# Kernel tuning notes

Hardware: AMD Instinct MI355X
Metric: run time of the kernel (lower is better)

The kernel has to match this reference:

```python
import jax, jax.numpy as jnp
import numpy as np

NB_CLASSES = 1024
SZ_EMBED = 128
N_SAMPLES = 262144
MRG = 0.1
ALPHA = 32.0


def l2_norm(x):
    # matches torch l2_norm: divide by sqrt(sum(x^2, dim=1) + 1e-12)
    return x / jnp.sqrt(jnp.sum(x * x, axis=1, keepdims=True) + 1e-12)


def setup_inputs() -> dict:
    key = jax.random.key(0)
    k1, k2, k3 = jax.random.split(key, 3)
    X = jax.random.normal(k1, (N_SAMPLES, SZ_EMBED), dtype=jnp.float32)
    proxies = jax.random.normal(k2, (NB_CLASSES, SZ_EMBED), dtype=jnp.float32)
    T = jax.random.randint(k3, (N_SAMPLES,), 0, NB_CLASSES)
    return {"X": X, "proxies": proxies, "T": T}


def reference(X, proxies, T):
    # cosine similarities: [N, C]
    cos = l2_norm(X) @ l2_norm(proxies).T
    # on-device one-hot replaces the numpy binarize roundtrip
    P_one_hot = jax.nn.one_hot(T, NB_CLASSES, dtype=cos.dtype)  # [N, C]
    pos_exp_w = jnp.exp(-ALPHA * (cos - MRG)) * P_one_hot
    neg_exp_w = jnp.exp(ALPHA * (cos + MRG)) * (1.0 - P_one_hot)
    P_sim_sum = pos_exp_w.sum(axis=0)  # [C]
    N_sim_sum = neg_exp_w.sum(axis=0)  # [C]
    num_valid = (P_one_hot.sum(axis=0) != 0).sum().astype(cos.dtype)
    pos_term = jnp.where(
        num_valid > 0,
        jnp.log1p(P_sim_sum).sum() / jnp.maximum(num_valid, 1.0),
        jnp.zeros((), cos.dtype),
    )
    neg_term = jnp.log1p(N_sim_sum).sum() / NB_CLASSES
    loss = pos_term + neg_term
    return jnp.stack([loss, pos_term, neg_term])
```

## Files before the change

### kernel.cpp

```cpp
#include <hip/hip_runtime.h>
#include <math.h>

#define NB_CLASSES 1024
#define SZ_EMBED 128
#define N_SAMPLES 262144
#define MTILE 64
#define CTILE 64
#define NBLOCKS (N_SAMPLES / MTILE)
#define XSTRIDE 136

typedef __bf16 v8bf __attribute__((ext_vector_type(8)));
typedef float v4f __attribute__((ext_vector_type(4)));
typedef float v2f __attribute__((ext_vector_type(2)));

#define EXP_A 46.16624130844683f
#define EXP_B 4.616624130844683f

#define SMEM_BYTES 36096

__device__ __forceinline__ unsigned short f2bf(float f) {
    union { float f; unsigned u; } v; v.f = f;
    unsigned u = v.u;
    unsigned rounding = 0x7FFFu + ((u >> 16) & 1u);
    return (unsigned short)((u + rounding) >> 16);
}
__device__ __forceinline__ float bfbits_lo(unsigned u) {
    union { unsigned u; float f; } v; v.u = u << 16; return v.f;
}
__device__ __forceinline__ float bfbits_hi(unsigned u) {
    union { unsigned u; float f; } v; v.u = u & 0xffff0000u; return v.f;
}

__global__ __launch_bounds__(256) void norm_proxies_kernel(
    const float* __restrict__ proxies, unsigned short* __restrict__ pn,
    float* __restrict__ pg) {
    if (blockIdx.x < 8) pg[blockIdx.x * 256 + threadIdx.x] = 0.f;
    int wv = threadIdx.x >> 6;
    int lane = threadIdx.x & 63;
    int row = blockIdx.x * 4 + wv;
    const float* src = proxies + (size_t)row * SZ_EMBED + lane * 2;
    float2 x = *(const float2*)src;
    float ss = x.x * x.x + x.y * x.y;
    #pragma unroll
    for (int off = 32; off; off >>= 1) ss += __shfl_xor(ss, off);
    float inv = rsqrtf(ss + 1e-12f);
    unsigned pk = (unsigned)f2bf(x.x * inv) | ((unsigned)f2bf(x.y * inv) << 16);
    *(unsigned*)(pn + (size_t)row * SZ_EMBED + lane * 2) = pk;
}

__global__ __launch_bounds__(256) void main_kernel(
    const float* __restrict__ X, const int* __restrict__ T,
    const unsigned short* __restrict__ Pn,
    float* __restrict__ partial_neg, float* __restrict__ pos_g,
    float* __restrict__ negd_g) {
    __shared__ __align__(16) char smem[SMEM_BYTES];
    unsigned short* xtile = (unsigned short*)smem;
    float (*psum)[4] = (float(*)[4])(smem + 17408);
    float (*dsum)[4] = (float(*)[4])(smem + 18432);
    int* tT = (int*)(smem + 19456);

    const int t = threadIdx.x;
    const int lane = t & 63;
    const int wv = t >> 6;
    const int quad = lane >> 4;
    const int l15 = lane & 15;
    const int sample_base = blockIdx.x * MTILE;
    const int row = t >> 2, part = t & 3;
    const char* PnB = (const char*)Pn;

#define STAGE(tc, b) do {                                                      \
        char* lb_ = smem + ((b) ? 0 : 19712) + wv * 4096;                      \
        _Pragma("unroll")                                                      \
        for (int c_ = 0; c_ < 4; ++c_) {                                       \
            int rw_ = c_ * 4 + (lane >> 4);                                    \
            const char* g_ = PnB + ((size_t)((tc) * 64 + wv * 16 + rw_)) * 256 \
                             + (((lane & 15) * 16) ^ ((rw_ & 7) << 4));        \
            __builtin_amdgcn_global_load_lds(                                  \
                (__attribute__((address_space(1))) const void*)g_,             \
                (__attribute__((address_space(3))) void*)(lb_ + c_ * 1024),    \
                16, 0, 0);                                                     \
        }                                                                      \
    } while (0)

    STAGE(0, 0);

    {
        const float4* src = (const float4*)(X + (size_t)(sample_base + row) * SZ_EMBED + part * 32);
        float4 r[8];
        float ss = 0.f;
        #pragma unroll
        for (int j = 0; j < 8; ++j) {
            r[j] = src[j];
            ss += r[j].x * r[j].x + r[j].y * r[j].y + r[j].z * r[j].z + r[j].w * r[j].w;
        }
        psum[row][part] = ss;
        if (t < MTILE) tT[t] = T[sample_base + t];
        __syncthreads();
        float inv = rsqrtf(psum[row][0] + psum[row][1] + psum[row][2] + psum[row][3] + 1e-12f);
        unsigned short* dst = xtile + row * XSTRIDE + part * 32;
        #pragma unroll
        for (int j = 0; j < 8; ++j) {
            uint2 pk;
            pk.x = (unsigned)f2bf(r[j].x * inv) | ((unsigned)f2bf(r[j].y * inv) << 16);
            pk.y = (unsigned)f2bf(r[j].z * inv) | ((unsigned)f2bf(r[j].w * inv) << 16);
            *(uint2*)(dst + j * 4) = pk;
        }
        int lbl = tT[row];
        const unsigned short* prow = Pn + (size_t)lbl * SZ_EMBED + part * 32;
        float d = 0.f;
        #pragma unroll
        for (int j = 0; j < 4; ++j) {
            uint4 pv = *(const uint4*)(prow + j * 8);
            float4 xa = r[2 * j], xb = r[2 * j + 1];
            d += bfbits_lo(pv.x) * xa.x + bfbits_hi(pv.x) * xa.y;
            d += bfbits_lo(pv.y) * xa.z + bfbits_hi(pv.y) * xa.w;
            d += bfbits_lo(pv.z) * xb.x + bfbits_hi(pv.z) * xb.y;
            d += bfbits_lo(pv.w) * xb.z + bfbits_hi(pv.w) * xb.w;
        }
        dsum[row][part] = d * inv;
        __syncthreads();
        if (part == 0) {
            int lbl2 = tT[row];
            float dd = dsum[row][0] + dsum[row][1] + dsum[row][2] + dsum[row][3];
            float dp = __builtin_amdgcn_exp2f(fmaf(dd, -EXP_A, EXP_B));
            float dn = __builtin_amdgcn_exp2f(fmaf(dd,  EXP_A, EXP_B));
            atomicAdd(&pos_g[lbl2], dp);
            atomicAdd(&negd_g[lbl2], dn);
        }
    }

    v8bf afrag[4][4];
    #pragma unroll
    for (int ri = 0; ri < 4; ++ri)
        #pragma unroll
        for (int kc = 0; kc < 4; ++kc)
            afrag[ri][kc] = *(const v8bf*)(xtile + (ri * 16 + l15) * XSTRIDE + kc * 32 + quad * 8);

    __syncthreads();

    float* nrow = partial_neg + (size_t)blockIdx.x * NB_CLASSES + wv * 16 + l15;
    const int bswz = ((l15 & 7) << 4);
    const int browoff = (wv * 16 + l15) * 256;

    #pragma unroll
    for (int ct = 0; ct < NB_CLASSES / CTILE; ++ct) {
        const int cur = ct & 1;
        if (ct < NB_CLASSES / CTILE - 1) {
            STAGE(ct + 1, cur ^ 1);
            asm volatile("s_waitcnt vmcnt(5)" ::: "memory");
        } else {
            asm volatile("s_waitcnt vmcnt(1)" ::: "memory");
        }
        __builtin_amdgcn_sched_barrier(0);

        const char* bbase = smem + (cur ? 0 : 19712) + browoff;
        v8bf bfrag[4];
        #pragma unroll
        for (int kc = 0; kc < 4; ++kc)
            bfrag[kc] = *(const v8bf*)(bbase + ((kc * 64 + quad * 16) ^ bswz));

        v4f zero = {0.f, 0.f, 0.f, 0.f};
        v4f acc[4] = {zero, zero, zero, zero};
        #pragma unroll
        for (int kc = 0; kc < 4; ++kc)
            #pragma unroll
            for (int ri = 0; ri < 4; ++ri)
                acc[ri] = __builtin_amdgcn_mfma_f32_16x16x32_bf16(afrag[ri][kc], bfrag[kc], acc[ri], 0, 0, 0);

        v2f e2[8];
        #pragma unroll
        for (int ri = 0; ri < 4; ++ri) {
            float a0 = __builtin_amdgcn_exp2f(fmaf(acc[ri][0], EXP_A, EXP_B));
            float a1 = __builtin_amdgcn_exp2f(fmaf(acc[ri][1], EXP_A, EXP_B));
            float a2 = __builtin_amdgcn_exp2f(fmaf(acc[ri][2], EXP_A, EXP_B));
            float a3 = __builtin_amdgcn_exp2f(fmaf(acc[ri][3], EXP_A, EXP_B));
            e2[ri * 2]     = (v2f){a0, a1};
            e2[ri * 2 + 1] = (v2f){a2, a3};
        }
        #pragma unroll
        for (int s2 = 4; s2; s2 >>= 1)
            #pragma unroll
            for (int j = 0; j < s2; ++j)
                e2[j] += e2[j + s2];
        float v = e2[0].x + e2[0].y;
        v += __shfl_xor(v, 16);
        v += __shfl_xor(v, 32);
        if (quad == 0) nrow[ct * CTILE] = v;
    }
#undef STAGE
}

__global__ __launch_bounds__(256) void row_reduce_kernel(float* __restrict__ partial_neg) {
    const int t = threadIdx.x;
    const int g = blockIdx.x >> 2, q = blockIdx.x & 3;
    float* base = partial_neg + (size_t)g * 64 * NB_CLASSES + q * 256 + t;
    float s = 0.f;
    #pragma unroll 8
    for (int r = 0; r < 64; ++r) s += base[(size_t)r * NB_CLASSES];
    base[0] = s;
}

__global__ __launch_bounds__(256) void finalize_kernel(
    const float* __restrict__ partial_neg, const float* __restrict__ pos_g,
    const float* __restrict__ negd_g, float* __restrict__ out) {
    int t = threadIdx.x;
    float4 ns = {0.f, 0.f, 0.f, 0.f};
    #pragma unroll 8
    for (int r = 0; r < 64; ++r) {
        float4 vn = *(const float4*)(partial_neg + (size_t)r * 64 * NB_CLASSES + 4 * t);
        ns.x += vn.x; ns.y += vn.y; ns.z += vn.z; ns.w += vn.w;
    }
    float4 nd = *(const float4*)(negd_g + 4 * t);
    ns.x -= nd.x; ns.y -= nd.y; ns.z -= nd.z; ns.w -= nd.w;
    float4 ps = *(const float4*)(pos_g + 4 * t);
    float lp_pos = log1pf(ps.x) + log1pf(ps.y) + log1pf(ps.z) + log1pf(ps.w);
    float lp_neg = log1pf(ns.x) + log1pf(ns.y) + log1pf(ns.z) + log1pf(ns.w);
    float valid = (ps.x != 0.f) + (ps.y != 0.f) + (ps.z != 0.f) + (ps.w != 0.f);
    #pragma unroll
    for (int off = 32; off; off >>= 1) {
        lp_pos += __shfl_xor(lp_pos, off);
        lp_neg += __shfl_xor(lp_neg, off);
        valid  += __shfl_xor(valid, off);
    }
    __shared__ float s[3][4];
    int wv = t >> 6, lane = t & 63;
    if (lane == 0) { s[0][wv] = lp_pos; s[1][wv] = lp_neg; s[2][wv] = valid; }
    __syncthreads();
    if (t == 0) {
        float P = s[0][0] + s[0][1] + s[0][2] + s[0][3];
        float Ng = s[1][0] + s[1][1] + s[1][2] + s[1][3];
        float V = s[2][0] + s[2][1] + s[2][2] + s[2][3];
        float pos_term = (V > 0.f) ? (P / fmaxf(V, 1.f)) : 0.f;
        float neg_term = Ng / (float)NB_CLASSES;
        out[0] = pos_term + neg_term;
        out[1] = pos_term;
        out[2] = neg_term;
    }
}

extern "C" void kernel_launch(void* const* d_in, const int* in_sizes, int n_in,
                              void* d_out, int out_size, void* d_ws, size_t ws_size,
                              hipStream_t stream) {
    const float* X = (const float*)d_in[0];
    const float* proxies = (const float*)d_in[1];
    const int* T = (const int*)d_in[2];
    float* out = (float*)d_out;

    char* ws = (char*)d_ws;
    unsigned short* Pn = (unsigned short*)ws;
    float* pos_g = (float*)(ws + (size_t)NB_CLASSES * SZ_EMBED * sizeof(unsigned short));
    float* negd_g = pos_g + NB_CLASSES;
    float* partial_neg = negd_g + NB_CLASSES;

    norm_proxies_kernel<<<NB_CLASSES / 4, 256, 0, stream>>>(proxies, Pn, pos_g);
    main_kernel<<<NBLOCKS, 256, 0, stream>>>(X, T, Pn, partial_neg, pos_g, negd_g);
    row_reduce_kernel<<<256, 256, 0, stream>>>(partial_neg);
    finalize_kernel<<<1, 256, 0, stream>>>(partial_neg, pos_g, negd_g, out);
}
```

Before: 279.7 us.

## Accumulate negative sums with global atomics and drop row-reduce kernel

Instead of writing per-block partial negative sums to a large buffer and reducing them in a separate kernel, each block atomically adds its per-class sums into a single 1024-entry global array. This removes a 16 MB intermediate write/read and one kernel launch, and simplifies finalize to a single load. The zero-init range is extended to cover the new accumulator. It trades that traffic for heavy atomic contention: thousands of blocks hit the same 1024 addresses, and summation order becomes nondeterministic.

```diff
diff --git a/kernel.cpp b/kernel.cpp
--- a/kernel.cpp
+++ b/kernel.cpp
@@ -34,7 +34,7 @@
 __global__ __launch_bounds__(256) void norm_proxies_kernel(
     const float* __restrict__ proxies, unsigned short* __restrict__ pn,
     float* __restrict__ pg) {
-    if (blockIdx.x < 8) pg[blockIdx.x * 256 + threadIdx.x] = 0.f;
+    if (blockIdx.x < 12) pg[blockIdx.x * 256 + threadIdx.x] = 0.f;
     int wv = threadIdx.x >> 6;
     int lane = threadIdx.x & 63;
     int row = blockIdx.x * 4 + wv;
@@ -51,7 +51,7 @@
 __global__ __launch_bounds__(256) void main_kernel(
     const float* __restrict__ X, const int* __restrict__ T,
     const unsigned short* __restrict__ Pn,
-    float* __restrict__ partial_neg, float* __restrict__ pos_g,
+    float* __restrict__ neg_total, float* __restrict__ pos_g,
     float* __restrict__ negd_g) {
     __shared__ __align__(16) char smem[SMEM_BYTES];
     unsigned short* xtile = (unsigned short*)smem;
@@ -138,7 +138,7 @@
 
     __syncthreads();
 
-    float* nrow = partial_neg + (size_t)blockIdx.x * NB_CLASSES + wv * 16 + l15;
+    float* ng = neg_total + wv * 16 + l15;
     const int bswz = ((l15 & 7) << 4);
     const int browoff = (wv * 16 + l15) * 256;
 
@@ -185,31 +185,16 @@
         float v = e2[0].x + e2[0].y;
         v += __shfl_xor(v, 16);
         v += __shfl_xor(v, 32);
-        if (quad == 0) nrow[ct * CTILE] = v;
+        if (quad == 0) atomicAdd(ng + ct * CTILE, v);
     }
 #undef STAGE
 }
 
-__global__ __launch_bounds__(256) void row_reduce_kernel(float* __restrict__ partial_neg) {
-    const int t = threadIdx.x;
-    const int g = blockIdx.x >> 2, q = blockIdx.x & 3;
-    float* base = partial_neg + (size_t)g * 64 * NB_CLASSES + q * 256 + t;
-    float s = 0.f;
-    #pragma unroll 8
-    for (int r = 0; r < 64; ++r) s += base[(size_t)r * NB_CLASSES];
-    base[0] = s;
-}
-
 __global__ __launch_bounds__(256) void finalize_kernel(
-    const float* __restrict__ partial_neg, const float* __restrict__ pos_g,
+    const float* __restrict__ neg_total, const float* __restrict__ pos_g,
     const float* __restrict__ negd_g, float* __restrict__ out) {
     int t = threadIdx.x;
-    float4 ns = {0.f, 0.f, 0.f, 0.f};
-    #pragma unroll 8
-    for (int r = 0; r < 64; ++r) {
-        float4 vn = *(const float4*)(partial_neg + (size_t)r * 64 * NB_CLASSES + 4 * t);
-        ns.x += vn.x; ns.y += vn.y; ns.z += vn.z; ns.w += vn.w;
-    }
+    float4 ns = *(const float4*)(neg_total + 4 * t);
     float4 nd = *(const float4*)(negd_g + 4 * t);
     ns.x -= nd.x; ns.y -= nd.y; ns.z -= nd.z; ns.w -= nd.w;
     float4 ps = *(const float4*)(pos_g + 4 * t);
@@ -250,10 +235,9 @@
     unsigned short* Pn = (unsigned short*)ws;
     float* pos_g = (float*)(ws + (size_t)NB_CLASSES * SZ_EMBED * sizeof(unsigned short));
     float* negd_g = pos_g + NB_CLASSES;
-    float* partial_neg = negd_g + NB_CLASSES;
+    float* neg_total = negd_g + NB_CLASSES;
 
     norm_proxies_kernel<<<NB_CLASSES / 4, 256, 0, stream>>>(proxies, Pn, pos_g);
-    main_kernel<<<NBLOCKS, 256, 0, stream>>>(X, T, Pn, partial_neg, pos_g, negd_g);
-    row_reduce_kernel<<<256, 256, 0, stream>>>(partial_neg);
-    finalize_kernel<<<1, 256, 0, stream>>>(partial_neg, pos_g, negd_g, out);
-}
+    main_kernel<<<NBLOCKS, 256, 0, stream>>>(X, T, Pn, neg_total, pos_g, negd_g);
+    finalize_kernel<<<1, 256, 0, stream>>>(neg_total, pos_g, negd_g, out);
+}
```

Measured after the change: 288.9 us. +3.3%, slower.
